# Kernel tuning notes

Hardware: AMD Instinct MI355X
Metric: run time of the kernel (lower is better)

## Reference

```python
import jax, jax.numpy as jnp
import numpy as np

B, D, DEPTH, C = 8192, 2048, 10, 1000
NUM_INNER = 2 ** DEPTH - 1   # 1023
NUM_LEAVES = 2 ** DEPTH      # 1024


def setup_inputs() -> dict:
    key = jax.random.key(0)
    k1, k2, k3, k4 = jax.random.split(key, 4)
    x = jax.random.normal(k1, (B, D), dtype=jnp.float32)
    # scale weights like a typical init so sigmoid isn't fully saturated
    W = jax.random.normal(k2, (D, NUM_INNER), dtype=jnp.float32) * 0.02
    b = jax.random.normal(k3, (NUM_INNER,), dtype=jnp.float32) * 0.02
    leaf_dist = jax.random.normal(k4, (NUM_LEAVES, C), dtype=jnp.float32)
    return {"x": x, "W": W, "b": b, "leaf_dist": leaf_dist}


def reference(x, W, b, leaf_dist):
    # inner node routing probabilities: [B, num_inner]
    decisions = jax.nn.sigmoid(x @ W + b)
    depth = int(np.log2(decisions.shape[1] + 1))
    pp = jnp.ones((x.shape[0], 1), dtype=x.dtype)  # path probs, starts at root
    for d in range(depth):  # small fixed loop over tree depth
        s, e = 2 ** d - 1, 2 ** (d + 1) - 1
        ld = decisions[:, s:e]                      # [B, 2^d]
        pp = jnp.concatenate([pp * ld, pp * (1.0 - ld)], axis=1)  # [B, 2^(d+1)]
        # faithful reproduction of the original's even/odd reordering
        pp = jnp.concatenate([pp[:, ::2], pp[:, 1::2]], axis=1)
    leaf_probs = jax.nn.softmax(leaf_dist, axis=1)  # [num_leaves, C]
    return pp @ leaf_probs                          # [B, C]
```

## Files before the change

### kernel.cpp

```cpp
#include <hip/hip_runtime.h>

typedef __attribute__((ext_vector_type(8))) unsigned short ushort8v;
typedef __attribute__((ext_vector_type(4))) unsigned short ushort4v;
typedef __attribute__((ext_vector_type(8))) __bf16 bf16x8;
typedef __attribute__((ext_vector_type(4))) float floatx4;

__device__ __forceinline__ unsigned short f2b(float f) {
    unsigned u = __float_as_uint(f);
    unsigned r = u + 0x7fffu + ((u >> 16) & 1u);
    return (unsigned short)(r >> 16);
}
__device__ __forceinline__ float b2f(unsigned short h) {
    return __uint_as_float(((unsigned)h) << 16);
}

__device__ __forceinline__ void gload16(const void* g, void* l) {
    __builtin_amdgcn_global_load_lds(
        (const __attribute__((address_space(1))) unsigned int*)g,
        (__attribute__((address_space(3))) unsigned int*)l,
        16, 0, 0);
}


__global__ __launch_bounds__(256) void prep_kernel(const float* __restrict__ x,
                                                   unsigned short* __restrict__ A2x,
                                                   const float* __restrict__ W,
                                                   unsigned short* __restrict__ B2w,
                                                   const float* __restrict__ ld_,
                                                   unsigned short* __restrict__ B2p) {
    __shared__ float tile[32 * 33];
    __shared__ float buf[1000];
    __shared__ float red[8];
    const int b = blockIdx.x, t = threadIdx.x;
    if (b < 2048) {
        const int mt = b >> 2, kq = (b & 3) * 64;
        const int l16 = t >> 4;
        const int sg  = t & 15;
        const float* xr = x + (size_t)(mt * 16 + l16) * 2048 + (size_t)(kq + sg * 4) * 8;
#pragma unroll
        for (int c = 0; c < 4; c++) {
            float4 v0 = *(const float4*)(xr + c * 8);
            float4 v1 = *(const float4*)(xr + c * 8 + 4);
            ushort8v o;
            o[0] = f2b(v0.x); o[1] = f2b(v0.y); o[2] = f2b(v0.z); o[3] = f2b(v0.w);
            o[4] = f2b(v1.x); o[5] = f2b(v1.y); o[6] = f2b(v1.z); o[7] = f2b(v1.w);
            const int kc = kq + sg * 4 + c;
            *(ushort8v*)(A2x + ((size_t)(mt * 256 + kc) * 16 + l16) * 8) = o;
        }
    } else if (b < 4096) {
        const int idx = b - 2048;
        const int n0 = (idx & 31) * 32, k0 = (idx >> 5) * 32;
        const int tx = t & 31, ty = t >> 5;
#pragma unroll
        for (int i = 0; i < 4; i++) {
            int k = k0 + ty + i * 8, n = n0 + tx;
            tile[(ty + i * 8) * 33 + tx] = (n < 1023) ? W[(size_t)k * 1023 + n] : 0.f;
        }
        __syncthreads();
        {
            const int tx2 = t & 31, ky = t >> 5;
            const int n = n0 + tx2;
            const int k = k0 + ky * 4;
            ushort4v o;
#pragma unroll
            for (int e = 0; e < 4; e++) o[e] = f2b(tile[(ky * 4 + e) * 33 + tx2]);
            size_t off = ((size_t)((n >> 4) * 256 + (k >> 3)) * 16 + (n & 15)) * 8 + (k & 7);
            *(ushort4v*)(B2w + off) = o;
        }
    } else {
        const int l0 = b - 4096;
        const float* r = ld_ + (size_t)l0 * 1000;
        float mx = -3.4e38f;
        for (int i = t; i < 1000; i += 256) { float v = r[i]; buf[i] = v; mx = fmaxf(mx, v); }
#pragma unroll
        for (int o = 32; o > 0; o >>= 1) mx = fmaxf(mx, __shfl_down(mx, o));
        if ((t & 63) == 0) red[t >> 6] = mx;
        __syncthreads();
        mx = fmaxf(fmaxf(red[0], red[1]), fmaxf(red[2], red[3]));
        float s = 0.f;
        for (int i = t; i < 1000; i += 256) { float e = __expf(buf[i] - mx); buf[i] = e; s += e; }
#pragma unroll
        for (int o = 32; o > 0; o >>= 1) s += __shfl_down(s, o);
        if ((t & 63) == 0) red[4 + (t >> 6)] = s;
        __syncthreads();
        float inv = 1.f / (red[4] + red[5] + red[6] + red[7]);
        for (int i = t; i < 1024; i += 256) {
            float pv = (i < 1000) ? buf[i] * inv : 0.f;
            size_t off = ((size_t)((i >> 4) * 128 + (l0 >> 3)) * 16 + (i & 15)) * 8 + (l0 & 7);
            B2p[off] = f2b(pv);
        }
    }
}

__global__ __launch_bounds__(256) void pp_kernel(const unsigned short* __restrict__ dec,
                                                 unsigned short* __restrict__ A2p) {
    __shared__ unsigned short dsh[8 * 1024];
    __shared__ float pa[8 * 1024];
    __shared__ float pb[8 * 1024];
    const int t = threadIdx.x;
    const int r0 = blockIdx.x * 8;
    {
        const ushort8v* src = (const ushort8v*)(dec + (size_t)r0 * 1024);
        ushort8v* dst = (ushort8v*)dsh;
        for (int g = t; g < 1024; g += 256) dst[g] = src[g];
    }
    __syncthreads();
    {
        const int r  = t >> 5;
        const int jb = (t & 31) * 2;
        const unsigned short* dr = &dsh[r * 1024];
#pragma unroll
        for (int e = 0; e < 2; e++) {
            int idx = jb + e;
            float fac[6];
#pragma unroll
            for (int dep = 5; dep >= 0; --dep) {
                const int half = 1 << dep;
                const int tt = idx >> dep;
                const int s  = idx & (half - 1);
                const int i2 = 2 * s + tt;
                const int u  = i2 >> dep;
                const int rr = i2 & (half - 1);
                const float dv = b2f(dr[half - 1 + rr]);
                fac[dep] = u ? (1.f - dv) : dv;
                idx = rr;
            }
            float prod = fac[0];
#pragma unroll
            for (int dep = 1; dep < 6; dep++) prod *= fac[dep];
            pa[r * 1024 + jb + e] = prod;
        }
    }
    __syncthreads();
    float* cur = pa; float* nxt = pb;
    for (int dep = 6; dep < 10; dep++) {
        const int half = 1 << dep;
        const int len  = half << 1;
        const int total = len << 3;
        for (int idx = t; idx < total; idx += 256) {
            const int r = idx >> (dep + 1);
            const int j = idx & (len - 1);
            int tt = j >> dep;
            int s  = j & (half - 1);
            int i2 = 2 * s + tt;
            int u  = i2 >> dep;
            int rr = i2 & (half - 1);
            float dv = b2f(dsh[r * 1024 + half - 1 + rr]);
            nxt[r * 1024 + j] = cur[r * 1024 + rr] * (u ? (1.f - dv) : dv);
        }
        __syncthreads();
        float* tmp = cur; cur = nxt; nxt = tmp;
    }
    {
        const int r  = t >> 5;
        const int jb = (t & 31) * 32;
        const int rrow = r0 + r;
        const float* cr = &cur[r * 1024];
        const size_t rbase = (size_t)(rrow >> 4) * 128 * 128 + (size_t)(rrow & 15) * 8;
#pragma unroll
        for (int g = 0; g < 8; g++) {
            const int j = jb + g * 4;
            ushort4v o;
            o[0] = f2b(cr[j]); o[1] = f2b(cr[j + 1]);
            o[2] = f2b(cr[j + 2]); o[3] = f2b(cr[j + 3]);
            size_t off = rbase + (size_t)(j >> 3) * 128 + (j & 7);
            *(ushort4v*)(A2p + off) = o;
        }
    }
}

#define VMW(N) asm volatile("s_waitcnt vmcnt(" #N ")" ::: "memory")

#define M1_STEP(ks_, CUR_, STG_, VM_, DOSTAGE_)                                       \
    {                                                                                 \
        if (DOSTAGE_) STAGE((ks_) + 2, (STG_));                                       \
        VMW(VM_);                                                                     \
        __builtin_amdgcn_s_barrier();                                                 \
        const unsigned short* lA = &lds[(CUR_)][0];                                   \
        const unsigned short* lB = &lds[(CUR_)][8192];                                \
        bf16x8 af[4], bv[4];                                                          \
        _Pragma("unroll")                                                             \
        for (int m2 = 0; m2 < 4; m2++)                                                \
            af[m2] = __builtin_bit_cast(bf16x8,                                       \
                *(const ushort8v*)&lA[((wr * 4 + m2) * 4 + quad) * 128 + l16 * 8]);   \
        _Pragma("unroll")                                                             \
        for (int n2 = 0; n2 < 4; n2++)                                                \
            bv[n2] = __builtin_bit_cast(bf16x8,                                       \
                *(const ushort8v*)&lB[((wc * 4 + n2) * 4 + quad) * 128 + l16 * 8]);   \
        asm volatile("s_waitcnt lgkmcnt(0)" ::: "memory");                            \
        __builtin_amdgcn_sched_barrier(0);                                            \
        __builtin_amdgcn_s_setprio(1);                                                \
        _Pragma("unroll")                                                             \
        for (int m2 = 0; m2 < 4; m2++)                                                \
            _Pragma("unroll")                                                         \
            for (int n2 = 0; n2 < 4; n2++)                                            \
                acc[m2][n2] = __builtin_amdgcn_mfma_f32_16x16x32_bf16(                \
                    af[m2], bv[n2], acc[m2][n2], 0, 0, 0);                            \
        __builtin_amdgcn_s_setprio(0);                                                \
        __builtin_amdgcn_s_barrier();                                                 \
    }

__global__ __launch_bounds__(512, 1) void gemm_m1(const unsigned short* __restrict__ A2,
                                                  const unsigned short* __restrict__ B2,
                                                  const float* __restrict__ bias,
                                                  unsigned short* __restrict__ obf) {
    constexpr int KC = 256;
    __shared__ unsigned short lds[3][12288];

    const int tid  = threadIdx.x;
    const int lane = tid & 63;
    const int wave = tid >> 6;
    const int quad = lane >> 4, l16 = lane & 15;
    const int wr = wave >> 1, wc = wave & 1;

    const int bid = blockIdx.x;
    const int xcd = bid & 7;
    const int j   = bid >> 3;
    const int bm  = xcd * 4 + (j & 3);
    const int bn  = j >> 2;

    const int cA  = tid >> 4;
    const int sub = (tid & 15) * 8;
    const unsigned short* gA0 = A2 + ((size_t)(bm * 16 + (cA >> 2))        * KC + (cA & 3)) * 128 + sub;
    const unsigned short* gA1 = A2 + ((size_t)(bm * 16 + ((cA + 32) >> 2)) * KC + (cA & 3)) * 128 + sub;
    const unsigned short* gB0 = B2 + ((size_t)(bn * 8  + (cA >> 2))        * KC + (cA & 3)) * 128 + sub;
    const int dA0 = cA * 128 + sub;
    const int dA1 = (cA + 32) * 128 + sub;
    const int dB0 = 8192 + cA * 128 + sub;

    floatx4 acc[4][4] = {};
    constexpr int nks = KC / 4;

    auto STAGE = [&](int ks, int b) {
        const size_t ko = (size_t)ks * 512;
        gload16(gA0 + ko, &lds[b][dA0]);
        gload16(gA1 + ko, &lds[b][dA1]);
        gload16(gB0 + ko, &lds[b][dB0]);
    };

    STAGE(0, 0); STAGE(1, 1);

    int c0 = 0, c1 = 1, c2 = 2;
    for (int ks = 0; ks < nks - 2; ++ks) {
        M1_STEP(ks, c0, c2, 6, true);
        int tmp = c0; c0 = c1; c1 = c2; c2 = tmp;
    }
    M1_STEP(nks - 2, c0, c2, 3, false);
    { int tmp = c0; c0 = c1; c1 = c2; c2 = tmp; }
    M1_STEP(nks - 1, c0, c2, 0, false);

    const int mt0 = bm * 16 + wr * 4;
    const int nt0 = bn * 8  + wc * 4;
#pragma unroll
    for (int n2 = 0; n2 < 4; n2++) {
        const int col = (nt0 + n2) * 16 + l16;
        const float bbias = (col < 1023) ? bias[col] : 0.f;
#pragma unroll
        for (int m2 = 0; m2 < 4; m2++) {
            const int row0 = (mt0 + m2) * 16 + quad * 4;
#pragma unroll
            for (int r = 0; r < 4; r++) {
                float sgm = 1.f / (1.f + __expf(-(acc[m2][n2][r] + bbias)));
                obf[(size_t)(row0 + r) * 1024 + col] = f2b(sgm);
            }
        }
    }
}

#define P4_STEP(ks_, b_, VM_, DOSTAGE_)                                             \
    {                                                                               \
        VMW(VM_);                                                                   \
        __builtin_amdgcn_s_barrier();                                               \
        __builtin_amdgcn_sched_barrier(0);                                          \
        const unsigned short* lA = &lds[(b_)][0];                                   \
        const unsigned short* lB = &lds[(b_)][4096];                                \
        bf16x8 af[4], bv[4];                                                        \
        _Pragma("unroll")                                                           \
        for (int m2 = 0; m2 < 4; m2++)                                              \
            af[m2] = __builtin_bit_cast(bf16x8,                                     \
                *(const ushort8v*)&lA[((wr * 4 + m2) * 4 + quad) * 128 + l16 * 8]); \
        _Pragma("unroll")                                                           \
        for (int n2 = 0; n2 < 4; n2++)                                              \
            bv[n2] = __builtin_bit_cast(bf16x8,                                     \
                *(const ushort8v*)&lB[((wc * 4 + n2) * 4 + quad) * 128 + l16 * 8]); \
        asm volatile("s_waitcnt lgkmcnt(0)" ::: "memory");                          \
        __builtin_amdgcn_sched_barrier(0);                                          \
        __builtin_amdgcn_s_barrier();                                               \
        __builtin_amdgcn_sched_barrier(0);                                          \
        if (DOSTAGE_) STAGE((ks_) + 4, (b_));                                       \
        __builtin_amdgcn_s_setprio(1);                                              \
        _Pragma("unroll")                                                           \
        for (int m2 = 0; m2 < 4; m2++)                                              \
            _Pragma("unroll")                                                       \
            for (int n2 = 0; n2 < 4; n2++)                                          \
                acc[m2][n2] = __builtin_amdgcn_mfma_f32_16x16x32_bf16(              \
                    af[m2], bv[n2], acc[m2][n2], 0, 0, 0);                          \
        __builtin_amdgcn_s_setprio(0);                                              \
    }

template <int KC>
__global__ __launch_bounds__(256, 2) void gemm_p4(const unsigned short* __restrict__ A2,
                                                  const unsigned short* __restrict__ B2,
                                                  float* __restrict__ of32, int ldo) {
    __shared__ unsigned short lds[4][8192];

    const int tid  = threadIdx.x;
    const int lane = tid & 63;
    const int wave = tid >> 6;
    const int quad = lane >> 4, l16 = lane & 15;
    const int wr = wave >> 1, wc = wave & 1;

    const int bid = blockIdx.x;
    const int xcd = bid & 7;
    const int j   = bid >> 3;
    const int bm  = xcd * 8 + (j & 7);
    const int bn  = j >> 3;

    const int c0  = tid >> 4;
    const int sub = (tid & 15) * 8;
    const unsigned short* gA0 = A2 + ((size_t)(bm * 8 + (c0 >> 2))        * KC + (c0 & 3)) * 128 + sub;
    const unsigned short* gA1 = A2 + ((size_t)(bm * 8 + ((c0 + 16) >> 2)) * KC + (c0 & 3)) * 128 + sub;
    const unsigned short* gB0 = B2 + ((size_t)(bn * 8 + (c0 >> 2))        * KC + (c0 & 3)) * 128 + sub;
    const unsigned short* gB1 = B2 + ((size_t)(bn * 8 + ((c0 + 16) >> 2)) * KC + (c0 & 3)) * 128 + sub;
    const int dA0 = c0 * 128 + sub;
    const int dA1 = (c0 + 16) * 128 + sub;
    const int dB0 = 4096 + c0 * 128 + sub;
    const int dB1 = 4096 + (c0 + 16) * 128 + sub;

    floatx4 acc[4][4] = {};
    constexpr int nks = KC / 4;

    auto STAGE = [&](int ks, int b) {
        const size_t ko = (size_t)ks * 512;
        gload16(gA0 + ko, &lds[b][dA0]);
        gload16(gA1 + ko, &lds[b][dA1]);
        gload16(gB0 + ko, &lds[b][dB0]);
        gload16(gB1 + ko, &lds[b][dB1]);
    };

    STAGE(0, 0); STAGE(1, 1); STAGE(2, 2); STAGE(3, 3);

    for (int ks = 0; ks < nks - 4; ++ks) {
        P4_STEP(ks, ks & 3, 12, true);
    }
    P4_STEP(nks - 4, (nks - 4) & 3, 12, false);
    P4_STEP(nks - 3, (nks - 3) & 3, 8,  false);
    P4_STEP(nks - 2, (nks - 2) & 3, 4,  false);
    P4_STEP(nks - 1, (nks - 1) & 3, 0,  false);

    const int mt0 = bm * 8 + wr * 4;
    const int nt0 = bn * 8 + wc * 4;
#pragma unroll
    for (int n2 = 0; n2 < 4; n2++) {
        const int col = (nt0 + n2) * 16 + l16;
#pragma unroll
        for (int m2 = 0; m2 < 4; m2++) {
            const int row0 = (mt0 + m2) * 16 + quad * 4;
#pragma unroll
            for (int r = 0; r < 4; r++) {
                if (col < 1000) of32[(size_t)(row0 + r) * ldo + col] = acc[m2][n2][r];
            }
        }
    }
}

extern "C" void kernel_launch(void* const* d_in, const int* in_sizes, int n_in,
                              void* d_out, int out_size, void* d_ws, size_t ws_size,
                              hipStream_t stream) {
    const float* x   = (const float*)d_in[0];
    const float* W   = (const float*)d_in[1];
    const float* b   = (const float*)d_in[2];
    const float* ldd = (const float*)d_in[3];
    float* out = (float*)d_out;

    char* ws = (char*)d_ws;
    unsigned short* A2x = (unsigned short*)(ws);
    unsigned short* A2p = (unsigned short*)(ws);
    unsigned short* B2w = (unsigned short*)(ws + 33554432);
    unsigned short* dec = (unsigned short*)(ws + 37748736);
    unsigned short* B2p = (unsigned short*)(ws + 54525952);

    prep_kernel<<<5120, 256, 0, stream>>>(x, A2x, W, B2w, ldd, B2p);
    gemm_m1<<<256, 512, 0, stream>>>(A2x, B2w, b, dec);
    pp_kernel<<<1024, 256, 0, stream>>>(dec, A2p);
    gemm_p4<128><<<512, 256, 0, stream>>>(A2p, B2p, out, 1000);
}
```

Before: 198.7 us.

## Fuse x fp32-to-bf16 conversion into first GEMM via fp32 LDS staging

Removes the separate pass in the prep kernel that converted x to a packed bf16 layout in workspace. The first GEMM now loads fp32 x directly into LDS using an XOR-swizzled layout and converts to bf16 in registers right before the MFMAs. The goal is to avoid writing and re-reading a 32MB intermediate. In exchange the GEMM moves twice as many bytes for A per k-step, uses more LDS, and spends extra VALU work on conversion. The block-to-tile mapping also changes from the XCD-aware scheme to a plain bn-fastest ordering.

```diff
diff --git a/kernel.cpp b/kernel.cpp
--- a/kernel.cpp
+++ b/kernel.cpp
@@ -13,7 +13,6 @@
 __device__ __forceinline__ float b2f(unsigned short h) {
     return __uint_as_float(((unsigned)h) << 16);
 }
-
 __device__ __forceinline__ void gload16(const void* g, void* l) {
     __builtin_amdgcn_global_load_lds(
         (const __attribute__((address_space(1))) unsigned int*)g,
@@ -21,10 +20,10 @@
         16, 0, 0);
 }
 
-
-__global__ __launch_bounds__(256) void prep_kernel(const float* __restrict__ x,
-                                                   unsigned short* __restrict__ A2x,
-                                                   const float* __restrict__ W,
+#define VMW(N) asm volatile("s_waitcnt vmcnt(" #N ")" ::: "memory")
+
+
+__global__ __launch_bounds__(256) void prep_kernel(const float* __restrict__ W,
                                                    unsigned short* __restrict__ B2w,
                                                    const float* __restrict__ ld_,
                                                    unsigned short* __restrict__ B2p) {
@@ -33,22 +32,7 @@
     __shared__ float red[8];
     const int b = blockIdx.x, t = threadIdx.x;
     if (b < 2048) {
-        const int mt = b >> 2, kq = (b & 3) * 64;
-        const int l16 = t >> 4;
-        const int sg  = t & 15;
-        const float* xr = x + (size_t)(mt * 16 + l16) * 2048 + (size_t)(kq + sg * 4) * 8;
-#pragma unroll
-        for (int c = 0; c < 4; c++) {
-            float4 v0 = *(const float4*)(xr + c * 8);
-            float4 v1 = *(const float4*)(xr + c * 8 + 4);
-            ushort8v o;
-            o[0] = f2b(v0.x); o[1] = f2b(v0.y); o[2] = f2b(v0.z); o[3] = f2b(v0.w);
-            o[4] = f2b(v1.x); o[5] = f2b(v1.y); o[6] = f2b(v1.z); o[7] = f2b(v1.w);
-            const int kc = kq + sg * 4 + c;
-            *(ushort8v*)(A2x + ((size_t)(mt * 256 + kc) * 16 + l16) * 8) = o;
-        }
-    } else if (b < 4096) {
-        const int idx = b - 2048;
+        const int idx = b;
         const int n0 = (idx & 31) * 32, k0 = (idx >> 5) * 32;
         const int tx = t & 31, ty = t >> 5;
 #pragma unroll
@@ -68,7 +52,7 @@
             *(ushort4v*)(B2w + off) = o;
         }
     } else {
-        const int l0 = b - 4096;
+        const int l0 = b - 2048;
         const float* r = ld_ + (size_t)l0 * 1000;
         float mx = -3.4e38f;
         for (int i = t; i < 1000; i += 256) { float v = r[i]; buf[i] = v; mx = fmaxf(mx, v); }
@@ -169,26 +153,34 @@
     }
 }
 
-#define VMW(N) asm volatile("s_waitcnt vmcnt(" #N ")" ::: "memory")
-
 #define M1_STEP(ks_, CUR_, STG_, VM_, DOSTAGE_)                                       \
     {                                                                                 \
         if (DOSTAGE_) STAGE((ks_) + 2, (STG_));                                       \
         VMW(VM_);                                                                     \
         __builtin_amdgcn_s_barrier();                                                 \
-        const unsigned short* lA = &lds[(CUR_)][0];                                   \
-        const unsigned short* lB = &lds[(CUR_)][8192];                                \
-        bf16x8 af[4], bv[4];                                                          \
+        const float* lA = ldsA[(CUR_)];                                               \
+        const unsigned short* lB = ldsB[(CUR_)];                                      \
+        float4 a0[4], a1[4]; bf16x8 bv[4];                                            \
         _Pragma("unroll")                                                             \
-        for (int m2 = 0; m2 < 4; m2++)                                                \
-            af[m2] = __builtin_bit_cast(bf16x8,                                       \
-                *(const ushort8v*)&lA[((wr * 4 + m2) * 4 + quad) * 128 + l16 * 8]);   \
+        for (int m2 = 0; m2 < 4; m2++) {                                              \
+            const int sb = (wr * 4 + m2) * 512 + l16 * 32;                            \
+            a0[m2] = *(const float4*)&lA[sb + (((quad * 2) ^ (l16 & 7)) * 4)];        \
+            a1[m2] = *(const float4*)&lA[sb + (((quad * 2 + 1) ^ (l16 & 7)) * 4)];    \
+        }                                                                             \
         _Pragma("unroll")                                                             \
         for (int n2 = 0; n2 < 4; n2++)                                                \
             bv[n2] = __builtin_bit_cast(bf16x8,                                       \
                 *(const ushort8v*)&lB[((wc * 4 + n2) * 4 + quad) * 128 + l16 * 8]);   \
         asm volatile("s_waitcnt lgkmcnt(0)" ::: "memory");                            \
         __builtin_amdgcn_sched_barrier(0);                                            \
+        bf16x8 af[4];                                                                 \
+        _Pragma("unroll")                                                             \
+        for (int m2 = 0; m2 < 4; m2++) {                                              \
+            af[m2][0] = (__bf16)a0[m2].x; af[m2][1] = (__bf16)a0[m2].y;               \
+            af[m2][2] = (__bf16)a0[m2].z; af[m2][3] = (__bf16)a0[m2].w;               \
+            af[m2][4] = (__bf16)a1[m2].x; af[m2][5] = (__bf16)a1[m2].y;               \
+            af[m2][6] = (__bf16)a1[m2].z; af[m2][7] = (__bf16)a1[m2].w;               \
+        }                                                                             \
         __builtin_amdgcn_s_setprio(1);                                                \
         _Pragma("unroll")                                                             \
         for (int m2 = 0; m2 < 4; m2++)                                                \
@@ -200,52 +192,53 @@
         __builtin_amdgcn_s_barrier();                                                 \
     }
 
-__global__ __launch_bounds__(512, 1) void gemm_m1(const unsigned short* __restrict__ A2,
+__global__ __launch_bounds__(512, 1) void gemm_m1(const float* __restrict__ x,
                                                   const unsigned short* __restrict__ B2,
                                                   const float* __restrict__ bias,
                                                   unsigned short* __restrict__ obf) {
     constexpr int KC = 256;
-    __shared__ unsigned short lds[3][12288];
-
-    const int tid  = threadIdx.x;
-    const int lane = tid & 63;
-    const int wave = tid >> 6;
+    __shared__ float          ldsA[3][8192];
+    __shared__ unsigned short ldsB[3][4096];
+
+    const int t    = threadIdx.x;
+    const int lane = t & 63;
+    const int wave = t >> 6;
     const int quad = lane >> 4, l16 = lane & 15;
     const int wr = wave >> 1, wc = wave & 1;
 
     const int bid = blockIdx.x;
-    const int xcd = bid & 7;
-    const int j   = bid >> 3;
-    const int bm  = xcd * 4 + (j & 3);
-    const int bn  = j >> 2;
-
-    const int cA  = tid >> 4;
-    const int sub = (tid & 15) * 8;
-    const unsigned short* gA0 = A2 + ((size_t)(bm * 16 + (cA >> 2))        * KC + (cA & 3)) * 128 + sub;
-    const unsigned short* gA1 = A2 + ((size_t)(bm * 16 + ((cA + 32) >> 2)) * KC + (cA & 3)) * 128 + sub;
-    const unsigned short* gB0 = B2 + ((size_t)(bn * 8  + (cA >> 2))        * KC + (cA & 3)) * 128 + sub;
-    const int dA0 = cA * 128 + sub;
-    const int dA1 = (cA + 32) * 128 + sub;
-    const int dB0 = 8192 + cA * 128 + sub;
+    const int bn  = bid & 7;
+    const int bm  = bid >> 3;
+
+    const float* srcA[4];
+#pragma unroll
+    for (int i = 0; i < 4; i++) {
+        const int li = i * 512 + t;
+        const int slab = li >> 7, row = (li >> 3) & 15, slot = li & 7;
+        srcA[i] = x + (size_t)(bm * 256 + slab * 16 + row) * 2048 + (slot ^ (row & 7)) * 4;
+    }
+    const int cB  = t >> 4;
+    const int sub = (t & 15) * 8;
+    const unsigned short* gB0 = B2 + ((size_t)(bn * 8 + (cB >> 2)) * KC + (cB & 3)) * 128 + sub;
+    const int dB0 = cB * 128 + sub;
 
     floatx4 acc[4][4] = {};
-    constexpr int nks = KC / 4;
+    constexpr int nks = 64;
 
     auto STAGE = [&](int ks, int b) {
-        const size_t ko = (size_t)ks * 512;
-        gload16(gA0 + ko, &lds[b][dA0]);
-        gload16(gA1 + ko, &lds[b][dA1]);
-        gload16(gB0 + ko, &lds[b][dB0]);
+#pragma unroll
+        for (int i = 0; i < 4; i++)
+            gload16(srcA[i] + ks * 32, &ldsA[b][(i * 512 + t) * 4]);
+        gload16(gB0 + (size_t)ks * 512, &ldsB[b][dB0]);
     };
 
     STAGE(0, 0); STAGE(1, 1);
-
     int c0 = 0, c1 = 1, c2 = 2;
     for (int ks = 0; ks < nks - 2; ++ks) {
-        M1_STEP(ks, c0, c2, 6, true);
+        M1_STEP(ks, c0, c2, 10, true);
         int tmp = c0; c0 = c1; c1 = c2; c2 = tmp;
     }
-    M1_STEP(nks - 2, c0, c2, 3, false);
+    M1_STEP(nks - 2, c0, c2, 5, false);
     { int tmp = c0; c0 = c1; c1 = c2; c2 = tmp; }
     M1_STEP(nks - 1, c0, c2, 0, false);
 
@@ -374,14 +367,13 @@
     float* out = (float*)d_out;
 
     char* ws = (char*)d_ws;
-    unsigned short* A2x = (unsigned short*)(ws);
     unsigned short* A2p = (unsigned short*)(ws);
     unsigned short* B2w = (unsigned short*)(ws + 33554432);
     unsigned short* dec = (unsigned short*)(ws + 37748736);
     unsigned short* B2p = (unsigned short*)(ws + 54525952);
 
-    prep_kernel<<<5120, 256, 0, stream>>>(x, A2x, W, B2w, ldd, B2p);
-    gemm_m1<<<256, 512, 0, stream>>>(A2x, B2w, b, dec);
+    prep_kernel<<<3072, 256, 0, stream>>>(W, B2w, ldd, B2p);
+    gemm_m1<<<256, 512, 0, stream>>>(x, B2w, b, dec);
     pp_kernel<<<1024, 256, 0, stream>>>(dec, A2p);
     gemm_p4<128><<<512, 256, 0, stream>>>(A2p, B2p, out, 1000);
 }
```

Result: slower. 246.5 us (+24.0%).

## Double K-step depth per stage and interleave staging with four MFMA phases

Applied to the files above, without the earlier changes.

The GEMM stage now covers 256 elements of K instead of 128, so LDS per buffer doubles and the main loop runs half as many iterations. Each step is split into four phases, each with its own barrier and prioritized MFMA group. The global-to-LDS prefetch loads for the next-next stage are spread across those phases instead of issued all at once. The aim is fewer barriers per unit of work and better overlap of memory issue with MFMA, at the cost of three times 48KB of LDS and more barriers inside each step.

```diff
diff --git a/kernel.cpp b/kernel.cpp
--- a/kernel.cpp
+++ b/kernel.cpp
@@ -13,13 +13,14 @@
 __device__ __forceinline__ float b2f(unsigned short h) {
     return __uint_as_float(((unsigned)h) << 16);
 }
-
 __device__ __forceinline__ void gload16(const void* g, void* l) {
     __builtin_amdgcn_global_load_lds(
         (const __attribute__((address_space(1))) unsigned int*)g,
         (__attribute__((address_space(3))) unsigned int*)l,
         16, 0, 0);
 }
+
+#define VMW(N) asm volatile("s_waitcnt vmcnt(" #N ")" ::: "memory")
 
 
 __global__ __launch_bounds__(256) void prep_kernel(const float* __restrict__ x,
@@ -169,35 +170,62 @@
     }
 }
 
-#define VMW(N) asm volatile("s_waitcnt vmcnt(" #N ")" ::: "memory")
-
-#define M1_STEP(ks_, CUR_, STG_, VM_, DOSTAGE_)                                       \
-    {                                                                                 \
-        if (DOSTAGE_) STAGE((ks_) + 2, (STG_));                                       \
-        VMW(VM_);                                                                     \
-        __builtin_amdgcn_s_barrier();                                                 \
-        const unsigned short* lA = &lds[(CUR_)][0];                                   \
-        const unsigned short* lB = &lds[(CUR_)][8192];                                \
-        bf16x8 af[4], bv[4];                                                          \
-        _Pragma("unroll")                                                             \
-        for (int m2 = 0; m2 < 4; m2++)                                                \
-            af[m2] = __builtin_bit_cast(bf16x8,                                       \
-                *(const ushort8v*)&lA[((wr * 4 + m2) * 4 + quad) * 128 + l16 * 8]);   \
-        _Pragma("unroll")                                                             \
-        for (int n2 = 0; n2 < 4; n2++)                                                \
-            bv[n2] = __builtin_bit_cast(bf16x8,                                       \
-                *(const ushort8v*)&lB[((wc * 4 + n2) * 4 + quad) * 128 + l16 * 8]);   \
-        asm volatile("s_waitcnt lgkmcnt(0)" ::: "memory");                            \
-        __builtin_amdgcn_sched_barrier(0);                                            \
-        __builtin_amdgcn_s_setprio(1);                                                \
-        _Pragma("unroll")                                                             \
-        for (int m2 = 0; m2 < 4; m2++)                                                \
-            _Pragma("unroll")                                                         \
-            for (int n2 = 0; n2 < 4; n2++)                                            \
-                acc[m2][n2] = __builtin_amdgcn_mfma_f32_16x16x32_bf16(                \
-                    af[m2], bv[n2], acc[m2][n2], 0, 0, 0);                            \
-        __builtin_amdgcn_s_setprio(0);                                                \
-        __builtin_amdgcn_s_barrier();                                                 \
+#define RD_A(m2_, kk_) __builtin_bit_cast(bf16x8, \
+    *(const ushort8v*)&lA[((wr * 4 + (m2_)) * 8 + (kk_) * 4 + quad) * 128 + l16 * 8])
+#define RD_B(n2_, kk_) __builtin_bit_cast(bf16x8, \
+    *(const ushort8v*)&lB[((wc * 4 + (n2_)) * 8 + (kk_) * 4 + quad) * 128 + l16 * 8])
+#define MM(AV_, m2_, n2_, BV_) acc[m2_][n2_] = \
+    __builtin_amdgcn_mfma_f32_16x16x32_bf16(AV_, BV_, acc[m2_][n2_], 0, 0, 0);
+#define STG_A(ks_, b_, i_) gload16(gA[i_] + (size_t)(ks_) * 1024, &lds[b_][(i_) * 4096 + dA]);
+#define STG_B(ks_, b_, i_) gload16(gB[i_] + (size_t)(ks_) * 1024, &lds[b_][(i_) * 4096 + dB]);
+
+#define PH_TAIL                                         \
+    __builtin_amdgcn_s_barrier();                       \
+    asm volatile("s_waitcnt lgkmcnt(0)" ::: "memory");  \
+    __builtin_amdgcn_sched_barrier(0);                  \
+    __builtin_amdgcn_s_setprio(1);
+
+#define PH_END                                          \
+    __builtin_amdgcn_s_setprio(0);                      \
+    __builtin_amdgcn_s_barrier();
+
+#define M8_STEP(ks_, CUR_, STG_, VM_, DOSTAGE_)                                   \
+    {                                                                             \
+        VMW(VM_);                                                                 \
+        __builtin_amdgcn_s_barrier();        \
+        const unsigned short* lA = &lds[(CUR_)][0];                               \
+        const unsigned short* lB = &lds[(CUR_)][16384];                           \
+        bf16x8 aE, aO, b0, b1, b2, b3;                                            \
+                                                       \
+        aE = RD_A(0, 0); aO = RD_A(1, 0);                                         \
+        b0 = RD_B(0, 0); b1 = RD_B(1, 0); b2 = RD_B(2, 0); b3 = RD_B(3, 0);       \
+        if (DOSTAGE_) { STG_A((ks_) + 2, STG_, 0); STG_A((ks_) + 2, STG_, 1); }   \
+        PH_TAIL                                                                   \
+        MM(aE, 0, 0, b0) MM(aE, 0, 1, b1) MM(aE, 0, 2, b2) MM(aE, 0, 3, b3)       \
+        MM(aO, 1, 0, b0) MM(aO, 1, 1, b1) MM(aO, 1, 2, b2) MM(aO, 1, 3, b3)       \
+        PH_END                                                                    \
+                                                       \
+        aE = RD_A(2, 0); aO = RD_A(3, 0);                                         \
+        if (DOSTAGE_) { STG_A((ks_) + 2, STG_, 2); STG_A((ks_) + 2, STG_, 3); }   \
+        PH_TAIL                                                                   \
+        MM(aE, 2, 0, b0) MM(aE, 2, 1, b1) MM(aE, 2, 2, b2) MM(aE, 2, 3, b3)       \
+        MM(aO, 3, 0, b0) MM(aO, 3, 1, b1) MM(aO, 3, 2, b2) MM(aO, 3, 3, b3)       \
+        PH_END                                                                    \
+                                                       \
+        aE = RD_A(0, 1); aO = RD_A(1, 1);                                         \
+        b0 = RD_B(0, 1); b1 = RD_B(1, 1); b2 = RD_B(2, 1); b3 = RD_B(3, 1);       \
+        if (DOSTAGE_) { STG_B((ks_) + 2, STG_, 0); }                              \
+        PH_TAIL                                                                   \
+        MM(aE, 0, 0, b0) MM(aE, 0, 1, b1) MM(aE, 0, 2, b2) MM(aE, 0, 3, b3)       \
+        MM(aO, 1, 0, b0) MM(aO, 1, 1, b1) MM(aO, 1, 2, b2) MM(aO, 1, 3, b3)       \
+        PH_END                                                                    \
+                                                       \
+        aE = RD_A(2, 1); aO = RD_A(3, 1);                                         \
+        if (DOSTAGE_) { STG_B((ks_) + 2, STG_, 1); }                              \
+        PH_TAIL                                                                   \
+        MM(aE, 2, 0, b0) MM(aE, 2, 1, b1) MM(aE, 2, 2, b2) MM(aE, 2, 3, b3)       \
+        MM(aO, 3, 0, b0) MM(aO, 3, 1, b1) MM(aO, 3, 2, b2) MM(aO, 3, 3, b3)       \
+        PH_END                                                                    \
     }
 
 __global__ __launch_bounds__(512, 1) void gemm_m1(const unsigned short* __restrict__ A2,
@@ -205,11 +233,11 @@
                                                   const float* __restrict__ bias,
                                                   unsigned short* __restrict__ obf) {
     constexpr int KC = 256;
-    __shared__ unsigned short lds[3][12288];
-
-    const int tid  = threadIdx.x;
-    const int lane = tid & 63;
-    const int wave = tid >> 6;
+    __shared__ unsigned short lds[3][24576];
+
+    const int t    = threadIdx.x;
+    const int lane = t & 63;
+    const int wave = t >> 6;
     const int quad = lane >> 4, l16 = lane & 15;
     const int wr = wave >> 1, wc = wave & 1;
 
@@ -219,35 +247,37 @@
     const int bm  = xcd * 4 + (j & 3);
     const int bn  = j >> 2;
 
-    const int cA  = tid >> 4;
-    const int sub = (tid & 15) * 8;
-    const unsigned short* gA0 = A2 + ((size_t)(bm * 16 + (cA >> 2))        * KC + (cA & 3)) * 128 + sub;
-    const unsigned short* gA1 = A2 + ((size_t)(bm * 16 + ((cA + 32) >> 2)) * KC + (cA & 3)) * 128 + sub;
-    const unsigned short* gB0 = B2 + ((size_t)(bn * 8  + (cA >> 2))        * KC + (cA & 3)) * 128 + sub;
-    const int dA0 = cA * 128 + sub;
-    const int dA1 = (cA + 32) * 128 + sub;
-    const int dB0 = 8192 + cA * 128 + sub;
+    const int cT  = t >> 4;
+    const int sub = (t & 15) * 8;
+    const unsigned short* gA[4];
+    const unsigned short* gB[2];
+#pragma unroll
+    for (int i = 0; i < 4; i++) {
+        const int c = i * 32 + cT;
+        gA[i] = A2 + ((size_t)(bm * 16 + (c >> 3)) * KC + (c & 7)) * 128 + sub;
+    }
+#pragma unroll
+    for (int i = 0; i < 2; i++) {
+        const int c = i * 32 + cT;
+        gB[i] = B2 + ((size_t)(bn * 8 + (c >> 3)) * KC + (c & 7)) * 128 + sub;
+    }
+    const int dA = cT * 128 + sub;
+    const int dB = 16384 + cT * 128 + sub;
 
     floatx4 acc[4][4] = {};
-    constexpr int nks = KC / 4;
-
-    auto STAGE = [&](int ks, int b) {
-        const size_t ko = (size_t)ks * 512;
-        gload16(gA0 + ko, &lds[b][dA0]);
-        gload16(gA1 + ko, &lds[b][dA1]);
-        gload16(gB0 + ko, &lds[b][dB0]);
-    };
-
-    STAGE(0, 0); STAGE(1, 1);
+    constexpr int nks = 32;
+
+    STG_A(0, 0, 0) STG_A(0, 0, 1) STG_A(0, 0, 2) STG_A(0, 0, 3) STG_B(0, 0, 0) STG_B(0, 0, 1)
+    STG_A(1, 1, 0) STG_A(1, 1, 1) STG_A(1, 1, 2) STG_A(1, 1, 3) STG_B(1, 1, 0) STG_B(1, 1, 1)
 
     int c0 = 0, c1 = 1, c2 = 2;
     for (int ks = 0; ks < nks - 2; ++ks) {
-        M1_STEP(ks, c0, c2, 6, true);
+        M8_STEP(ks, c0, c2, 6, true);
         int tmp = c0; c0 = c1; c1 = c2; c2 = tmp;
     }
-    M1_STEP(nks - 2, c0, c2, 3, false);
+    M8_STEP(nks - 2, c0, c2, 6, false);
     { int tmp = c0; c0 = c1; c1 = c2; c2 = tmp; }
-    M1_STEP(nks - 1, c0, c2, 0, false);
+    M8_STEP(nks - 1, c0, c2, 0, false);
 
     const int mt0 = bm * 16 + wr * 4;
     const int nt0 = bn * 8  + wc * 4;
```

Result: no change. 200.4 us (+0.8%).

## Widen first GEMM to 16 waves with doubled K per stage

Applied to the files above, without the earlier changes.

The x@W GEMM kernel moves from 512 to 1024 threads per block, with 16 waves arranged 4x4, each owning a 4x2 tile of 16x16 accumulators instead of 4x4. Each pipeline stage now loads twice as much K (two 32-wide sub-steps), so there are half as many barrier-separated steps, and LDS per buffer doubles. The intent is more waves to hide latency and fewer synchronizations per K. In exchange, each wave does less MFMA work per LDS fragment load, and the larger LDS footprint may limit residency. The launch bound of (1024,4) is also unlikely to be achievable given the LDS size.

```diff
diff --git a/kernel.cpp b/kernel.cpp
--- a/kernel.cpp
+++ b/kernel.cpp
@@ -13,13 +13,14 @@
 __device__ __forceinline__ float b2f(unsigned short h) {
     return __uint_as_float(((unsigned)h) << 16);
 }
-
 __device__ __forceinline__ void gload16(const void* g, void* l) {
     __builtin_amdgcn_global_load_lds(
         (const __attribute__((address_space(1))) unsigned int*)g,
         (__attribute__((address_space(3))) unsigned int*)l,
         16, 0, 0);
 }
+
+#define VMW(N) asm volatile("s_waitcnt vmcnt(" #N ")" ::: "memory")
 
 
 __global__ __launch_bounds__(256) void prep_kernel(const float* __restrict__ x,
@@ -169,49 +170,49 @@
     }
 }
 
-#define VMW(N) asm volatile("s_waitcnt vmcnt(" #N ")" ::: "memory")
-
-#define M1_STEP(ks_, CUR_, STG_, VM_, DOSTAGE_)                                       \
-    {                                                                                 \
-        if (DOSTAGE_) STAGE((ks_) + 2, (STG_));                                       \
-        VMW(VM_);                                                                     \
-        __builtin_amdgcn_s_barrier();                                                 \
-        const unsigned short* lA = &lds[(CUR_)][0];                                   \
-        const unsigned short* lB = &lds[(CUR_)][8192];                                \
-        bf16x8 af[4], bv[4];                                                          \
-        _Pragma("unroll")                                                             \
-        for (int m2 = 0; m2 < 4; m2++)                                                \
-            af[m2] = __builtin_bit_cast(bf16x8,                                       \
-                *(const ushort8v*)&lA[((wr * 4 + m2) * 4 + quad) * 128 + l16 * 8]);   \
-        _Pragma("unroll")                                                             \
-        for (int n2 = 0; n2 < 4; n2++)                                                \
-            bv[n2] = __builtin_bit_cast(bf16x8,                                       \
-                *(const ushort8v*)&lB[((wc * 4 + n2) * 4 + quad) * 128 + l16 * 8]);   \
-        asm volatile("s_waitcnt lgkmcnt(0)" ::: "memory");                            \
-        __builtin_amdgcn_sched_barrier(0);                                            \
-        __builtin_amdgcn_s_setprio(1);                                                \
-        _Pragma("unroll")                                                             \
-        for (int m2 = 0; m2 < 4; m2++)                                                \
-            _Pragma("unroll")                                                         \
-            for (int n2 = 0; n2 < 4; n2++)                                            \
-                acc[m2][n2] = __builtin_amdgcn_mfma_f32_16x16x32_bf16(                \
-                    af[m2], bv[n2], acc[m2][n2], 0, 0, 0);                            \
-        __builtin_amdgcn_s_setprio(0);                                                \
-        __builtin_amdgcn_s_barrier();                                                 \
-    }
-
-__global__ __launch_bounds__(512, 1) void gemm_m1(const unsigned short* __restrict__ A2,
-                                                  const unsigned short* __restrict__ B2,
-                                                  const float* __restrict__ bias,
-                                                  unsigned short* __restrict__ obf) {
+#define R16A(m2_, kk_) __builtin_bit_cast(bf16x8, \
+    *(const ushort8v*)&lA[((wr * 4 + (m2_)) * 8 + (kk_) * 4 + quad) * 128 + l16 * 8])
+#define R16B(n2_, kk_) __builtin_bit_cast(bf16x8, \
+    *(const ushort8v*)&lB[((wc * 2 + (n2_)) * 8 + (kk_) * 4 + quad) * 128 + l16 * 8])
+#define MM16(AV_, m2_, n2_, BV_) acc[m2_][n2_] = \
+    __builtin_amdgcn_mfma_f32_16x16x32_bf16(AV_, BV_, acc[m2_][n2_], 0, 0, 0);
+
+#define M16_STEP(ks_, CUR_, STG_, VM_, DOSTAGE_)                                  \
+    {                                                                             \
+        if (DOSTAGE_) STAGE((ks_) + 2, (STG_));                                   \
+        VMW(VM_);                                                                 \
+        __builtin_amdgcn_s_barrier();                                             \
+        const unsigned short* lA = &lds[(CUR_)][0];                               \
+        const unsigned short* lB = &lds[(CUR_)][16384];                           \
+        _Pragma("unroll")                                                         \
+        for (int kk = 0; kk < 2; kk++) {                                          \
+            bf16x8 a0 = R16A(0, kk), a1 = R16A(1, kk);                            \
+            bf16x8 a2 = R16A(2, kk), a3 = R16A(3, kk);                            \
+            bf16x8 b0 = R16B(0, kk), b1 = R16B(1, kk);                            \
+            asm volatile("s_waitcnt lgkmcnt(0)" ::: "memory");                    \
+            __builtin_amdgcn_sched_barrier(0);                                    \
+            __builtin_amdgcn_s_setprio(1);                                        \
+            MM16(a0, 0, 0, b0) MM16(a0, 0, 1, b1)                                 \
+            MM16(a1, 1, 0, b0) MM16(a1, 1, 1, b1)                                 \
+            MM16(a2, 2, 0, b0) MM16(a2, 2, 1, b1)                                 \
+            MM16(a3, 3, 0, b0) MM16(a3, 3, 1, b1)                                 \
+            __builtin_amdgcn_s_setprio(0);                                        \
+        }                                                                         \
+        __builtin_amdgcn_s_barrier();                                             \
+    }
+
+__global__ __launch_bounds__(1024, 4) void gemm_m1(const unsigned short* __restrict__ A2,
+                                                   const unsigned short* __restrict__ B2,
+                                                   const float* __restrict__ bias,
+                                                   unsigned short* __restrict__ obf) {
     constexpr int KC = 256;
-    __shared__ unsigned short lds[3][12288];
-
-    const int tid  = threadIdx.x;
-    const int lane = tid & 63;
-    const int wave = tid >> 6;
+    __shared__ unsigned short lds[3][24576];
+
+    const int t    = threadIdx.x;
+    const int lane = t & 63;
+    const int wave = t >> 6;
     const int quad = lane >> 4, l16 = lane & 15;
-    const int wr = wave >> 1, wc = wave & 1;
+    const int wr = wave >> 2, wc = wave & 3;
 
     const int bid = blockIdx.x;
     const int xcd = bid & 7;
@@ -219,40 +220,43 @@
     const int bm  = xcd * 4 + (j & 3);
     const int bn  = j >> 2;
 
-    const int cA  = tid >> 4;
-    const int sub = (tid & 15) * 8;
-    const unsigned short* gA0 = A2 + ((size_t)(bm * 16 + (cA >> 2))        * KC + (cA & 3)) * 128 + sub;
-    const unsigned short* gA1 = A2 + ((size_t)(bm * 16 + ((cA + 32) >> 2)) * KC + (cA & 3)) * 128 + sub;
-    const unsigned short* gB0 = B2 + ((size_t)(bn * 8  + (cA >> 2))        * KC + (cA & 3)) * 128 + sub;
-    const int dA0 = cA * 128 + sub;
-    const int dA1 = (cA + 32) * 128 + sub;
-    const int dB0 = 8192 + cA * 128 + sub;
-
-    floatx4 acc[4][4] = {};
-    constexpr int nks = KC / 4;
+    const int cT  = t >> 4;
+    const int sub = (t & 15) * 8;
+    const unsigned short* gA[2];
+#pragma unroll
+    for (int i = 0; i < 2; i++) {
+        const int c = i * 64 + cT;
+        gA[i] = A2 + ((size_t)(bm * 16 + (c >> 3)) * KC + (c & 7)) * 128 + sub;
+    }
+    const unsigned short* gB0 = B2 + ((size_t)(bn * 8 + (cT >> 3)) * KC + (cT & 7)) * 128 + sub;
+    const int dA = t * 8;
+    const int dB = 16384 + t * 8;
+
+    floatx4 acc[4][2] = {};
+    constexpr int nks = 32;
 
     auto STAGE = [&](int ks, int b) {
-        const size_t ko = (size_t)ks * 512;
-        gload16(gA0 + ko, &lds[b][dA0]);
-        gload16(gA1 + ko, &lds[b][dA1]);
-        gload16(gB0 + ko, &lds[b][dB0]);
+        const size_t ko = (size_t)ks * 1024;
+        gload16(gA[0] + ko, &lds[b][dA]);
+        gload16(gA[1] + ko, &lds[b][8192 + dA]);
+        gload16(gB0 + ko, &lds[b][dB]);
     };
 
     STAGE(0, 0); STAGE(1, 1);
 
     int c0 = 0, c1 = 1, c2 = 2;
     for (int ks = 0; ks < nks - 2; ++ks) {
-        M1_STEP(ks, c0, c2, 6, true);
+        M16_STEP(ks, c0, c2, 6, true);
         int tmp = c0; c0 = c1; c1 = c2; c2 = tmp;
     }
-    M1_STEP(nks - 2, c0, c2, 3, false);
+    M16_STEP(nks - 2, c0, c2, 3, false);
     { int tmp = c0; c0 = c1; c1 = c2; c2 = tmp; }
-    M1_STEP(nks - 1, c0, c2, 0, false);
+    M16_STEP(nks - 1, c0, c2, 0, false);
 
     const int mt0 = bm * 16 + wr * 4;
-    const int nt0 = bn * 8  + wc * 4;
-#pragma unroll
-    for (int n2 = 0; n2 < 4; n2++) {
+    const int nt0 = bn * 8  + wc * 2;
+#pragma unroll
+    for (int n2 = 0; n2 < 2; n2++) {
         const int col = (nt0 + n2) * 16 + l16;
         const float bbias = (col < 1023) ? bias[col] : 0.f;
 #pragma unroll
@@ -381,7 +385,7 @@
     unsigned short* B2p = (unsigned short*)(ws + 54525952);
 
     prep_kernel<<<5120, 256, 0, stream>>>(x, A2x, W, B2w, ldd, B2p);
-    gemm_m1<<<256, 512, 0, stream>>>(A2x, B2w, b, dec);
+    gemm_m1<<<256, 1024, 0, stream>>>(A2x, B2w, b, dec);
     pp_kernel<<<1024, 256, 0, stream>>>(dec, A2p);
     gemm_p4<128><<<512, 256, 0, stream>>>(A2p, B2p, out, 1000);
 }
```

Result: no change. 199.1 us (+0.2%).
